# Performance work log

Measured on AMD Instinct MI355X. Metric: run time of the kernel, lower is better.

Reference implementation:

```python
import jax, jax.numpy as jnp
import numpy as np

S_DIM = 4096
N_NODES = 4096
N_EDGES = 32768


def _coarsen(ei_np, N):
    """Integer-only greedy coarsening, faithful to MNGRAPH.forward's while-loop.
    Returns (select order, flattened neighbor indices, segment ids, per-hub
    neighbor counts, forward-fill indices replicating the stale-M behavior for
    empty neighborhoods, and the remapped final edge_index)."""
    ei = ei_np.astype(np.int64).copy()
    I = np.bincount(ei[0], minlength=N)
    O = np.bincount(ei[1], minlength=N)
    order = np.argsort(-(I + O), kind='stable')  # torch.argsort(D, descending=True)
    visits = np.zeros(N, dtype=bool)
    select = []
    nbr_idx, nbr_seg, counts = [], [], []
    while order.size > 0:
        node = int(order[0])
        select.append(node)
        visits[node] = True
        # H = unique neighbors of node in the CURRENT (rewritten) edge_index
        H = np.unique(np.concatenate([ei[1][ei[0] == node], ei[0][ei[1] == node]]))
        visits[H] = True
        order = order[~visits[order]]
        # rewrite: endpoints in H that are not already-selected hubs -> node
        Hn = H[~np.isin(H, np.asarray(select, dtype=np.int64))]
        ei[np.isin(ei, Hn)] = node
        ei = ei[:, ei[0] != ei[1]]  # drop self-loops
        # append reversed edges that are not already present (pair-code isin
        # == the original O(E^2) all/any comparison, computed efficiently)
        code = ei[0] * N + ei[1]
        rcode = ei[1] * N + ei[0]
        new = ~np.isin(rcode, code)
        ei = np.concatenate([ei, ei[::-1][:, new]], axis=1)
        k = len(select) - 1
        nbr_idx.append(H)
        nbr_seg.append(np.full(H.shape[0], k, dtype=np.int64))
        counts.append(H.shape[0])
    select = np.asarray(select, dtype=np.int64)
    sort_sel = np.sort(select)
    ei_out = np.searchsorted(sort_sel, ei)  # compact node ids
    counts = np.asarray(counts, dtype=np.int64)
    # forward-fill: when H is empty the original appends the previous (stale) M
    fill = np.arange(select.shape[0])
    for i in range(select.shape[0]):
        if counts[i] == 0:
            fill[i] = fill[i - 1] if i > 0 else 0
    nbr = np.concatenate(nbr_idx) if nbr_idx else np.zeros(0, np.int64)
    seg = np.concatenate(nbr_seg) if nbr_seg else np.zeros(0, np.int64)
    return select, nbr, seg, counts, fill, ei_out


def setup_inputs() -> dict:
    key = jax.random.key(0)
    k1, k2, k3, k4 = jax.random.split(key, 4)
    x = jax.random.normal(k1, (N_NODES, S_DIM), dtype=jnp.float32)
    edge_index = jax.random.randint(k2, (2, N_EDGES), 0, N_NODES, dtype=jnp.int64)
    bound = float(np.sqrt(6.0 / (1.0 + S_DIM)))  # xavier_uniform on (1, S)
    W1 = jax.random.uniform(k3, (S_DIM,), jnp.float32, -bound, bound)
    W2 = jax.random.uniform(k4, (S_DIM,), jnp.float32, -bound, bound)
    B1 = jnp.zeros((S_DIM,), jnp.float32)
    B2 = jnp.zeros((S_DIM,), jnp.float32)
    return {"x": x, "edge_index": edge_index, "W1": W1, "W2": W2, "B1": B1, "B2": B2}


def reference(x, edge_index, W1, W2, B1, B2):
    N = x.shape[0]
    sel, nbr, seg, counts, fill, ei_out = _coarsen(np.asarray(edge_index), N)
    K = sel.shape[0]
    # Dn = x[n]*W1+B1 for every neighbor of every hub; per-hub mean via segment_sum
    Dn = x[jnp.asarray(nbr)] * W1 + B1                      # [T, S]
    sums = jax.ops.segment_sum(Dn, jnp.asarray(seg), num_segments=K)
    denom = jnp.maximum(jnp.asarray(counts), 1).astype(x.dtype)[:, None]
    mean_Dn = sums / denom                                  # [K, S]
    Dv = x[jnp.asarray(sel)] * W2 + B2                      # [K, S]
    END = jnp.concatenate([Dv, mean_Dn], axis=1)            # [K, 2S]
    END = END[jnp.asarray(fill)]                            # stale-M replication
    return END, jnp.asarray(ei_out)
```

## Files before the change

### kernel.cpp

```cpp
#include <hip/hip_runtime.h>
#include <hip/hip_bf16.h>

#define NT 1024
#define NNODES 4096
#define ECAP 65536

__global__ __launch_bounds__(256)
void zeroBM(int4* __restrict__ bm) {
    bm[(size_t)blockIdx.x * 256 + threadIdx.x] = make_int4(0, 0, 0, 0);
}

__device__ __forceinline__ int blockScanExcl(int v, int* s_w, int* total) {
    const int tid  = threadIdx.x;
    const int lane = tid & 63;
    const int wv   = tid >> 6;
    int x = v;
#pragma unroll
    for (int off = 1; off < 64; off <<= 1) {
        int t = __shfl_up(x, off, 64);
        if (lane >= off) x += t;
    }
    if (lane == 63) s_w[wv] = x;
    __syncthreads();
    if (tid < 16) {
        int y = s_w[tid];
#pragma unroll
        for (int off = 1; off < 16; off <<= 1) {
            int t = __shfl_up(y, off, 16);
            if (tid >= off) y += t;
        }
        s_w[tid] = y;
    }
    __syncthreads();
    int base = wv ? s_w[wv - 1] : 0;
    int tot  = s_w[15];
    __syncthreads();
    *total = tot;
    return base + x - v;
}

__global__ __launch_bounds__(NT, 1)
void phaseA1(const int* __restrict__ ei, int E0,
             int* __restrict__ U, int* __restrict__ V,
             unsigned int* __restrict__ BM,
             int* __restrict__ NBR, int* __restrict__ OTH,
             int* __restrict__ ORDV, int* __restrict__ ROFFG, int* __restrict__ RENDG,
             int* __restrict__ HAND)
{
    __shared__ unsigned short s_order[NNODES];
    __shared__ unsigned char  s_vis[NNODES];
    __shared__ unsigned char  s_rank[NNODES];
    __shared__ unsigned int   s_hb[NNODES / 32];
    __shared__ int s_roff[NNODES];
    __shared__ int s_rend[NNODES];
    __shared__ int s_tmp[NNODES];
    __shared__ int s_mat[64][65];
    __shared__ int s_w[16];
    __shared__ int s_bc[16];

    const int tid = threadIdx.x;

    for (int i = tid; i < NNODES; i += NT) { s_vis[i] = 0; s_tmp[i] = 0; }
    for (int i = tid; i < NNODES / 32; i += NT) s_hb[i] = 0;
    if (tid < 16) s_bc[tid] = 0;
    __syncthreads();

    for (int i = tid; i < E0; i += NT)
        if (ei[2 * i + 1] != 0) s_bc[9] = 1;
    __syncthreads();
    const int is64 = !s_bc[9];

    for (int e = tid; e < E0; e += NT) {
        int uu = ei[is64 ? 2 * e : e];
        int vv = ei[is64 ? 2 * (E0 + e) : (E0 + e)];
        U[e] = uu; V[e] = vv;
        atomicAdd(&s_tmp[uu], 1);
        atomicAdd(&s_tmp[vv], 1);
    }
    __syncthreads();
    for (int n = tid; n < NNODES; n += NT) atomicMax(&s_bc[7], s_tmp[n]);
    __syncthreads();
    const int maxd = s_bc[7];

    if (maxd < 64) {
        const int wv = tid >> 6, lane = tid & 63;
        const unsigned long long ltm = (1ull << lane) - 1ull;
        for (int g = wv; g < 64; g += 16) {
            int n = g * 64 + lane;
            int d = s_tmp[n];
            int rk = 0;
            for (int dd = 0; dd < 64; ++dd) {
                unsigned long long bal = __ballot(d == dd);
                if (lane == 0) s_mat[dd][g] = __popcll(bal);
                if (d == dd) rk = __popcll(bal & ltm);
            }
            s_rank[n] = (unsigned char)rk;
        }
        __syncthreads();
        if (tid < 64) {
            int run = 0;
            for (int g = 0; g < 64; ++g) { int t = s_mat[tid][g]; s_mat[tid][g] = run; run += t; }
            s_mat[tid][64] = run;
        }
        __syncthreads();
        if (tid < 64) {
            int x = s_mat[tid][64];
#pragma unroll
            for (int off = 1; off < 64; off <<= 1) {
                int t = __shfl_up(x, off, 64);
                if (tid >= off) x += t;
            }
            int T = __shfl(x, 63, 64);
            s_mat[tid][64] = T - x;
        }
        __syncthreads();
        for (int g = wv; g < 64; g += 16) {
            int n = g * 64 + lane;
            int d = s_tmp[n];
            int pos = s_mat[d][64] + s_mat[d][g] + (int)s_rank[n];
            s_order[pos] = (unsigned short)n;
        }
        __syncthreads();
    } else {
        for (int d = maxd; d >= 0; --d) {
            int n0 = tid * 4;
            int f0 = (s_tmp[n0] == d), f1 = (s_tmp[n0 + 1] == d);
            int f2 = (s_tmp[n0 + 2] == d), f3 = (s_tmp[n0 + 3] == d);
            int tot;
            int off = blockScanExcl(f0 + f1 + f2 + f3, s_w, &tot);
            int idx = s_bc[4] + off;
            if (f0) s_order[idx++] = (unsigned short)n0;
            if (f1) s_order[idx++] = (unsigned short)(n0 + 1);
            if (f2) s_order[idx++] = (unsigned short)(n0 + 2);
            if (f3) s_order[idx++] = (unsigned short)(n0 + 3);
            __syncthreads();
            if (tid == 0) s_bc[4] += tot;
            __syncthreads();
        }
    }

    if (tid == 0) {
        int nd = s_order[0];
        s_bc[0] = nd; s_vis[nd] = 1;
    }
    __syncthreads();
    {
        const int node = s_bc[0];
        for (int e = tid; e < E0; e += NT) {
            int uu = U[e], vv = V[e];
            if (uu == node) {
                int w = vv; unsigned m = 1u << (w & 31);
                unsigned old = atomicOr(&s_hb[w >> 5], m);
                if (!(old & m)) { int i = atomicAdd(&s_bc[2], 1); s_tmp[i] = w; s_vis[w] = 1; }
            }
            if (vv == node) {
                int w = uu; unsigned m = 1u << (w & 31);
                unsigned old = atomicOr(&s_hb[w >> 5], m);
                if (!(old & m)) { int i = atomicAdd(&s_bc[2], 1); s_tmp[i] = w; s_vis[w] = 1; }
            }
        }
        __syncthreads();
        for (int e = tid; e < E0; e += NT) {
            int uu = U[e];
            if (uu != node && ((s_hb[uu >> 5] >> (uu & 31)) & 1)) U[e] = node;
            int vv = V[e];
            if (vv != node && ((s_hb[vv >> 5] >> (vv & 31)) & 1)) V[e] = node;
        }
        __syncthreads();
    }

    for (int e = tid; e < E0; e += NT) {
        int uu = U[e], vv = V[e];
        if (uu != vv) {
            unsigned code = ((unsigned)uu << 12) | (unsigned)vv;
            atomicOr(&BM[code >> 5], 1u << (code & 31));
        }
    }
    __syncthreads();
    for (int t0 = 0; t0 < E0; t0 += NT * 32) {
        unsigned fm = 0u;
        const int base = t0 + tid * 32;
        for (int j = 0; j < 32; ++j) {
            int e = base + j;
            if (e < E0) {
                int uu = U[e], vv = V[e];
                if (uu != vv) {
                    unsigned rc = ((unsigned)vv << 12) | (unsigned)uu;
                    unsigned old = atomicOr(&BM[rc >> 5], 0u);
                    if (!((old >> (rc & 31)) & 1u)) fm |= (1u << j);
                }
            }
        }
        int tot;
        int off = blockScanExcl(__popc(fm), s_w, &tot);
        int r = s_bc[5] + off;
        unsigned m = fm;
        while (m) {
            int j = __ffs((int)m) - 1; m &= m - 1;
            int e = base + j;
            U[E0 + r] = V[e]; V[E0 + r] = U[e];
            ++r;
        }
        __syncthreads();
        if (tid == 0) s_bc[5] += tot;
        __syncthreads();
    }
    const int E1 = E0 + s_bc[5];

    for (int n = tid; n < NNODES; n += NT) s_roff[n] = 0;
    __syncthreads();
    for (int e = tid; e < E1; e += NT) {
        int uu = U[e], vv = V[e];
        if (uu != vv) atomicAdd(&s_roff[uu], 1);
    }
    __syncthreads();
    {
        int n0 = tid * 4;
        int c0 = s_roff[n0], c1 = s_roff[n0 + 1], c2 = s_roff[n0 + 2], c3 = s_roff[n0 + 3];
        int tot;
        int off = blockScanExcl(c0 + c1 + c2 + c3, s_w, &tot);
        int st = off;
        s_roff[n0] = st;     s_rend[n0] = st;     st += c0;
        s_roff[n0 + 1] = st; s_rend[n0 + 1] = st; st += c1;
        s_roff[n0 + 2] = st; s_rend[n0 + 2] = st; st += c2;
        s_roff[n0 + 3] = st; s_rend[n0 + 3] = st;
    }
    __syncthreads();
    for (int e = tid; e < E1; e += NT) {
        int uu = U[e], vv = V[e];
        if (uu != vv) {
            int p = atomicAdd(&s_rend[uu], 1);
            OTH[p] = vv;
        }
    }
    __syncthreads();
    {
        const int cnt0 = s_bc[2];
        for (int i = tid; i < cnt0; i += NT) NBR[i] = s_tmp[i];
    }
    for (int i = tid; i < NNODES; i += NT) {
        int nd = (int)s_order[i];
        ORDV[i]  = nd | (s_vis[nd] ? 0x8000 : 0);
        ROFFG[i] = s_roff[i];
        RENDG[i] = s_rend[i];
    }
    if (tid == 0) { HAND[0] = E1; HAND[1] = s_bc[2]; HAND[2] = s_bc[0]; }
}

__global__ __launch_bounds__(64, 1)
void phaseA2(const int* __restrict__ OTH, int* __restrict__ NBR,
             const int* __restrict__ ORDV, const int* __restrict__ ROFFG,
             const int* __restrict__ RENDG, const int* __restrict__ HAND,
             int* __restrict__ SEL, int* __restrict__ CNTS,
             int* __restrict__ NST, int* __restrict__ FIL, int* __restrict__ SC,
             int* __restrict__ LABG, int* __restrict__ RNKG)
{
    __shared__ unsigned short s_ord[NNODES];
    __shared__ unsigned int   s_visbits[NNODES / 32];
    __shared__ unsigned int   s_meta[NNODES];
    __shared__ unsigned short s_so[NNODES];
    __shared__ int s_cnt[NNODES];
    __shared__ int s_stamp[NNODES];
    __shared__ int s_roff[NNODES];
    __shared__ int s_rend[NNODES];

    const int ln = threadIdx.x;
    const unsigned long long ltm = (1ull << ln) - 1ull;
    const int cnt0 = HAND[1], hub0 = HAND[2];
    volatile int* vstamp = s_stamp;

    for (int i = ln; i < NNODES / 32; i += 64) s_visbits[i] = 0u;
    for (int i = ln; i < NNODES; i += 64) {
        int ov = ORDV[i];
        int nd = ov & 0x7FFF;
        s_ord[i] = (unsigned short)nd;
        s_meta[nd] = ((unsigned)i << 16) | (unsigned)nd;
        s_roff[i] = ROFFG[i];
        s_rend[i] = RENDG[i];
        s_stamp[i] = 0; s_cnt[i] = 0;
        if (ov & 0x8000) atomicOr(&s_visbits[i >> 5], 1u << (i & 31));
    }
    if (ln == 0) {
        s_meta[hub0] = (unsigned)hub0 | 0x8000u;
        s_so[0] = (unsigned short)hub0;
        s_cnt[0] = cnt0;
    }

    int nc = cnt0;
    int k = 1;

    unsigned lo = 0u, hi = 0u;
    auto reload = [&]() { lo = ~s_visbits[ln]; hi = ~s_visbits[ln + 64]; };
    auto extract = [&]() -> int {
        unsigned long long b = __ballot(lo != 0u);
        if (b) {
            int sl = __ffsll((long long)b) - 1;
            unsigned ww = __shfl(lo, sl, 64);
            if (ln == sl) lo &= lo - 1;
            return sl * 32 + (__ffs((int)ww) - 1);
        }
        b = __ballot(hi != 0u);
        if (b) {
            int sl = __ffsll((long long)b) - 1;
            unsigned ww = __shfl(hi, sl, 64);
            if (ln == sl) hi &= hi - 1;
            return 2048 + sl * 32 + (__ffs((int)ww) - 1);
        }
        return -1;
    };

    auto commitNew = [&](unsigned g, int w, bool nw, unsigned long long bal,
                         unsigned relv) {
        if (nw) {
            NBR[nc + __popcll(bal & ltm)] = w;
            int slot = (int)(g >> 16);
            atomicOr(&s_visbits[slot >> 5], 1u << (slot & 31));
            if (!(g & 0x8000u)) s_meta[w] = relv;
        }
        nc += __popcll(bal);
    };

    auto procFast = [&](int hub, int hslot, int o, unsigned g) {
        const unsigned relv = ((unsigned)hslot << 16) | (unsigned)hub | 0x8000u;
        int w = (o >= 0) ? (int)(g & 0x7FFFu) : hub;
        bool valid = (o >= 0) && (w != hub);
        if (valid) vstamp[w] = ln;
        int r = valid ? vstamp[w] : -1;
        bool nw = valid && (r == ln);
        unsigned long long bal = __ballot(nw);
        commitNew(g, w, nw, bal, relv);
    };

    auto procSlow = [&](int hub, int hslot, int rb, int re, int o0) {
        const unsigned relv = ((unsigned)hslot << 16) | (unsigned)hub | 0x8000u;
        const int key = k << 6;
        int o = o0;
        for (int s0 = rb; s0 < re; s0 += 64) {
            unsigned g = (o >= 0) ? s_meta[o] : 0u;
            int w = (o >= 0) ? (int)(g & 0x7FFFu) : hub;
            bool cnd = (w != hub);
            int old = key;
            if (cnd) old = atomicMax(&s_stamp[w], key);
            bool nw = cnd && (old < key);
            unsigned long long bal = __ballot(nw);
            commitNew(g, w, nw, bal, relv);
            int s1 = s0 + 64;
            o = (s1 + ln < re) ? OTH[s1 + ln] : -1;
        }
    };

    for (;;) {
        reload();
        int sl0 = extract();
        if (sl0 < 0) break;
        int sl1 = extract(), sl2 = -1, sl3 = -1;
        if (sl1 >= 0) { sl2 = extract(); if (sl2 >= 0) sl3 = extract(); }

        int c0 = (int)s_ord[sl0];
        int c1 = (sl1 >= 0) ? (int)s_ord[sl1] : -1;
        int c2 = (sl2 >= 0) ? (int)s_ord[sl2] : -1;
        int c3 = (sl3 >= 0) ? (int)s_ord[sl3] : -1;

        {
            int ms = (ln == 0) ? sl0 : (ln == 1) ? sl1 : (ln == 2) ? sl2 : sl3;
            if (ln < 4 && ms >= 0) atomicOr(&s_visbits[ms >> 5], 1u << (ms & 31));
        }

        int rb0 = s_roff[c0], re0 = s_rend[c0];
        int rb1 = 0, re1 = 0, rb2 = 0, re2 = 0, rb3 = 0, re3 = 0;
        if (c1 >= 0) { rb1 = s_roff[c1]; re1 = s_rend[c1]; }
        if (c2 >= 0) { rb2 = s_roff[c2]; re2 = s_rend[c2]; }
        if (c3 >= 0) { rb3 = s_roff[c3]; re3 = s_rend[c3]; }
        int v0 = (rb0 + ln < re0) ? OTH[rb0 + ln] : -1;
        int v1 = (c1 >= 0 && rb1 + ln < re1) ? OTH[rb1 + ln] : -1;
        int v2 = (c2 >= 0 && rb2 + ln < re2) ? OTH[rb2 + ln] : -1;
        int v3 = (c3 >= 0 && rb3 + ln < re3) ? OTH[rb3 + ln] : -1;

        if (ln == 0) {
            s_meta[c0] = ((unsigned)sl0 << 16) | (unsigned)c0 | 0x8000u;
            s_so[k] = (unsigned short)c0;
        }
        {
            unsigned g0 = (v0 >= 0) ? s_meta[v0] : 0u;
            int begin = nc;
            if (re0 - rb0 <= 64) procFast(c0, sl0, v0, g0);
            else                 procSlow(c0, sl0, rb0, re0, v0);
            if (ln == 0) s_cnt[k] = nc - begin;
            k++;
        }
        if (c1 >= 0) {
            unsigned m1 = s_meta[c1];
            unsigned g1 = (v1 >= 0) ? s_meta[v1] : 0u;
            if ((int)(m1 & 0x7FFFu) == c1) {
                if (ln == 0) {
                    s_meta[c1] = ((unsigned)sl1 << 16) | (unsigned)c1 | 0x8000u;
                    s_so[k] = (unsigned short)c1;
                }
                int begin = nc;
                if (re1 - rb1 <= 64) procFast(c1, sl1, v1, g1);
                else                 procSlow(c1, sl1, rb1, re1, v1);
                if (ln == 0) s_cnt[k] = nc - begin;
                k++;
            }
        }
        if (c2 >= 0) {
            unsigned m2 = s_meta[c2];
            unsigned g2 = (v2 >= 0) ? s_meta[v2] : 0u;
            if ((int)(m2 & 0x7FFFu) == c2) {
                if (ln == 0) {
                    s_meta[c2] = ((unsigned)sl2 << 16) | (unsigned)c2 | 0x8000u;
                    s_so[k] = (unsigned short)c2;
                }
                int begin = nc;
                if (re2 - rb2 <= 64) procFast(c2, sl2, v2, g2);
                else                 procSlow(c2, sl2, rb2, re2, v2);
                if (ln == 0) s_cnt[k] = nc - begin;
                k++;
            }
        }
        if (c3 >= 0) {
            unsigned m3 = s_meta[c3];
            unsigned g3 = (v3 >= 0) ? s_meta[v3] : 0u;
            if ((int)(m3 & 0x7FFFu) == c3) {
                if (ln == 0) {
                    s_meta[c3] = ((unsigned)sl3 << 16) | (unsigned)c3 | 0x8000u;
                    s_so[k] = (unsigned short)c3;
                }
                int begin = nc;
                if (re3 - rb3 <= 64) procFast(c3, sl3, v3, g3);
                else                 procSlow(c3, sl3, rb3, re3, v3);
                if (ln == 0) s_cnt[k] = nc - begin;
                k++;
            }
        }
    }
    const int K = k;

    {
        int base = 0;
        for (int c = 0; c < NNODES / 64; ++c) {
            int n = c * 64 + ln;
            unsigned mv = s_meta[n];
            int f = ((mv & 0x8000u) != 0u) && ((int)(mv & 0x7FFFu) == n);
            unsigned long long b = __ballot(f);
            s_stamp[n] = base + __popcll(b & ltm);
            base += __popcll(b);
        }
    }
    {
        int nb = 0;
        for (int c = 0; c * 64 < K; ++c) {
            int i = c * 64 + ln;
            int cv = (i < K) ? s_cnt[i] : 0;
            int x = cv;
#pragma unroll
            for (int off = 1; off < 64; off <<= 1) {
                int t = __shfl_up(x, off, 64);
                if (ln >= off) x += t;
            }
            if (i < K) { NST[i] = nb + x - cv; CNTS[i] = cv; SEL[i] = (int)s_so[i]; }
            nb += __shfl(x, 63, 64);
        }
    }
    {
        int carry = 0;
        for (int c = 0; c * 64 < K; ++c) {
            int i = c * 64 + ln;
            int f = (i < K) && (s_cnt[i] > 0);
            unsigned long long b = __ballot(f);
            unsigned long long m = b & ((ln == 63) ? ~0ull : ((1ull << (ln + 1)) - 1ull));
            int fil = m ? (c * 64 + 63 - __clzll(m)) : carry;
            if (i < K) FIL[i] = fil;
            carry = b ? (c * 64 + 63 - __clzll(b)) : carry;
        }
    }
    if (ln == 0) SC[0] = K;
    for (int i = ln; i < NNODES; i += 64) {
        LABG[i] = (int)(s_meta[i] & 0x7FFFu);
        RNKG[i] = s_stamp[i];
    }
}

__global__ __launch_bounds__(NT, 1)
void phaseA3(const int* __restrict__ U, const int* __restrict__ V,
             const int* __restrict__ LABG, const int* __restrict__ RNKG,
             const int* __restrict__ HAND, int* __restrict__ SC,
             int* __restrict__ TMP, float* __restrict__ out)
{
    __shared__ unsigned short l_lab[NNODES];
    __shared__ int l_rnk[NNODES];
    __shared__ int s_w[16];
    __shared__ int s_base[1];

    const int tid = threadIdx.x;
    for (int i = tid; i < NNODES; i += NT) {
        l_lab[i] = (unsigned short)LABG[i];
        l_rnk[i] = RNKG[i];
    }
    if (tid == 0) s_base[0] = 0;
    __syncthreads();

    const int E1 = HAND[0];
    const int K  = SC[0];
    const size_t obase = (size_t)K * 8192;

    for (int t0 = 0; t0 < E1; t0 += NT * 64) {
        unsigned long long fm = 0ull;
        const int base = t0 + tid * 64;
        if (base + 64 <= E1) {
            const int4* U4 = (const int4*)(U + base);
            const int4* V4 = (const int4*)(V + base);
#pragma unroll
            for (int q = 0; q < 16; ++q) {
                int4 a = U4[q], b = V4[q];
                int j = q * 4;
                if ((int)l_lab[a.x] != (int)l_lab[b.x]) fm |= 1ull << j;
                if ((int)l_lab[a.y] != (int)l_lab[b.y]) fm |= 1ull << (j + 1);
                if ((int)l_lab[a.z] != (int)l_lab[b.z]) fm |= 1ull << (j + 2);
                if ((int)l_lab[a.w] != (int)l_lab[b.w]) fm |= 1ull << (j + 3);
            }
        } else {
            for (int j = 0; j < 64; ++j) {
                int e = base + j;
                if (e < E1) {
                    if ((int)l_lab[U[e]] != (int)l_lab[V[e]]) fm |= 1ull << j;
                }
            }
        }
        int tot;
        int off = blockScanExcl(__popcll(fm), s_w, &tot);
        int r = s_base[0] + off;
        unsigned long long m = fm;
        while (m) {
            int j = __ffsll((long long)m) - 1; m &= m - 1;
            int e = base + j;
            out[obase + (size_t)r] = (float)l_rnk[(int)l_lab[U[e]]];
            TMP[r] = l_rnk[(int)l_lab[V[e]]];
            ++r;
        }
        __syncthreads();
        if (tid == 0) s_base[0] += tot;
        __syncthreads();
    }
    const int Ef = s_base[0];
    if (tid == 0) SC[1] = Ef;
    for (int r = tid; r < Ef; r += NT)
        out[obase + (size_t)Ef + (size_t)r] = (float)TMP[r];
}

__global__ __launch_bounds__(256, 4)
void phaseB(const float* __restrict__ x,
            const float* __restrict__ W1, const float* __restrict__ W2,
            const float* __restrict__ B1, const float* __restrict__ B2,
            const int* __restrict__ NBR, const int* __restrict__ SEL,
            const int* __restrict__ CNTS, const int* __restrict__ NST,
            const int* __restrict__ FIL, const int* __restrict__ SC,
            float* __restrict__ out)
{
    const int K = SC[0];
    const int k = blockIdx.x;
    if (k >= K) return;
    const int kk   = FIL[k];
    const int node = SEL[kk];
    const int cnt  = CNTS[kk];
    const int st   = NST[kk];
    const int tid  = threadIdx.x;
    const float4* x4 = (const float4*)x;

    float4 acc[4];
#pragma unroll
    for (int j = 0; j < 4; j++) acc[j] = make_float4(0.f, 0.f, 0.f, 0.f);

    for (int r = 0; r < cnt; ++r) {
        const float4* row = x4 + (size_t)NBR[st + r] * 1024;
#pragma unroll
        for (int j = 0; j < 4; j++) {
            float4 t = row[tid + j * 256];
            acc[j].x += t.x; acc[j].y += t.y; acc[j].z += t.z; acc[j].w += t.w;
        }
    }

    const float fc  = (float)cnt;
    const float inv = 1.0f / (float)(cnt > 1 ? cnt : 1);
    const float4* xr = x4 + (size_t)node * 1024;
    float4* o4 = (float4*)(out + (size_t)k * 8192);

#pragma unroll
    for (int j = 0; j < 4; j++) {
        int c = tid + j * 256;
        float4 w1 = ((const float4*)W1)[c], b1 = ((const float4*)B1)[c];
        float4 w2 = ((const float4*)W2)[c], b2 = ((const float4*)B2)[c];
        float4 xv = xr[c];
        float4 pd, pm;
        pd.x = xv.x * w2.x + b2.x;
        pd.y = xv.y * w2.y + b2.y;
        pd.z = xv.z * w2.z + b2.z;
        pd.w = xv.w * w2.w + b2.w;
        pm.x = (acc[j].x * w1.x + fc * b1.x) * inv;
        pm.y = (acc[j].y * w1.y + fc * b1.y) * inv;
        pm.z = (acc[j].z * w1.z + fc * b1.z) * inv;
        pm.w = (acc[j].w * w1.w + fc * b1.w) * inv;
        o4[c] = pd;
        o4[1024 + c] = pm;
    }
}

extern "C" void kernel_launch(void* const* d_in, const int* in_sizes, int n_in,
                              void* d_out, int out_size, void* d_ws, size_t ws_size,
                              hipStream_t stream)
{
    const float* x  = (const float*)d_in[0];
    const int*   ei = (const int*)d_in[1];
    const float* W1 = (const float*)d_in[2];
    const float* W2 = (const float*)d_in[3];
    const float* B1 = (const float*)d_in[4];
    const float* B2 = (const float*)d_in[5];
    const int E0 = in_sizes[1] / 2;

    char* w = (char*)d_ws;
    int* U = (int*)w;
    int* V = U + ECAP;
    unsigned int* BM = (unsigned int*)(V + ECAP);
    int* OTH = (int*)BM;
    int* NBR = OTH + 2 * ECAP;
    int* TMP = NBR + 2 * ECAP;
    char* meta = (char*)BM + (2u << 20);
    int* SEL   = (int*)meta;
    int* CNTS  = SEL  + NNODES;
    int* NST   = CNTS + NNODES;
    int* FIL   = NST  + NNODES;
    int* SC    = FIL  + NNODES;
    int* ORDV  = SC   + 16;
    int* ROFFG = ORDV + NNODES;
    int* RENDG = ROFFG + NNODES;
    int* LABG  = RENDG + NNODES;
    int* RNKG  = LABG + NNODES;
    int* HAND  = RNKG + NNODES;
    float* out = (float*)d_out;

    hipLaunchKernelGGL(zeroBM, dim3(512), dim3(256), 0, stream, (int4*)BM);

    hipLaunchKernelGGL(phaseA1, dim3(1), dim3(NT), 0, stream,
                       ei, E0, U, V, BM, NBR, OTH, ORDV, ROFFG, RENDG, HAND);
    hipLaunchKernelGGL(phaseA2, dim3(1), dim3(64), 0, stream,
                       OTH, NBR, ORDV, ROFFG, RENDG, HAND,
                       SEL, CNTS, NST, FIL, SC, LABG, RNKG);
    hipLaunchKernelGGL(phaseA3, dim3(1), dim3(NT), 0, stream,
                       U, V, LABG, RNKG, HAND, SC, TMP, out);
    hipLaunchKernelGGL(phaseB, dim3(NNODES), dim3(256), 0, stream,
                       x, W1, W2, B1, B2, NBR, SEL, CNTS, NST, FIL, SC, out);
}
```

Measured before the change: 1.005 ms.

## Software-pipeline hub candidate selection in octets with next-batch prefetch

The greedy coarsening loop now pulls eight candidate hubs per iteration instead of four. While the current octet is being processed, it already extracts the next octet's candidates from the visited bitmap and loads their adjacency ranges and first neighbor ids. This is meant to hide LDS and global load latency in the serial single-wave loop behind useful work. In exchange it uses more registers, and it depends on the existing per-candidate s_meta check to reject prefetched nodes that the current octet has just claimed.

```diff
diff --git a/kernel.cpp b/kernel.cpp
--- a/kernel.cpp
+++ b/kernel.cpp
@@ -290,7 +290,6 @@
     int k = 1;
 
     unsigned lo = 0u, hi = 0u;
-    auto reload = [&]() { lo = ~s_visbits[ln]; hi = ~s_visbits[ln + 64]; };
     auto extract = [&]() -> int {
         unsigned long long b = __ballot(lo != 0u);
         if (b) {
@@ -349,91 +348,66 @@
         }
     };
 
+    int nsl0=-1,nsl1=-1,nsl2=-1,nsl3=-1,nsl4=-1,nsl5=-1,nsl6=-1,nsl7=-1;
+    int ncd0=-1,ncd1=-1,ncd2=-1,ncd3=-1,ncd4=-1,ncd5=-1,ncd6=-1,ncd7=-1;
+    int nrb0=0,nrb1=0,nrb2=0,nrb3=0,nrb4=0,nrb5=0,nrb6=0,nrb7=0;
+    int nre0=0,nre1=0,nre2=0,nre3=0,nre4=0,nre5=0,nre6=0,nre7=0;
+    int nv0=-1,nv1=-1,nv2=-1,nv3=-1,nv4=-1,nv5=-1,nv6=-1,nv7=-1;
+
+#define PF_ONE(i) \
+    ncd##i = (nsl##i >= 0) ? (int)s_ord[nsl##i] : -1; \
+    nrb##i = 0; nre##i = 0; \
+    if (ncd##i >= 0) { nrb##i = s_roff[ncd##i]; nre##i = s_rend[ncd##i]; } \
+    nv##i = (ncd##i >= 0 && nrb##i + ln < nre##i) ? OTH[nrb##i + ln] : -1;
+
+#define PREFETCH_OCTET() do { \
+    lo = ~s_visbits[ln]; hi = ~s_visbits[ln + 64]; \
+    nsl0 = extract(); nsl1 = extract(); nsl2 = extract(); nsl3 = extract(); \
+    nsl4 = extract(); nsl5 = extract(); nsl6 = extract(); nsl7 = extract(); \
+    { int ms = (ln==0)?nsl0:(ln==1)?nsl1:(ln==2)?nsl2:(ln==3)?nsl3: \
+               (ln==4)?nsl4:(ln==5)?nsl5:(ln==6)?nsl6:nsl7; \
+      if (ln < 8 && ms >= 0) atomicOr(&s_visbits[ms >> 5], 1u << (ms & 31)); } \
+    PF_ONE(0) PF_ONE(1) PF_ONE(2) PF_ONE(3) PF_ONE(4) PF_ONE(5) PF_ONE(6) PF_ONE(7) \
+} while (0)
+
+#define DO_CAND(CC, SLI, RBI, REI, VI) \
+    if (CC >= 0) { \
+        unsigned mm = s_meta[CC]; \
+        unsigned gg = (VI >= 0) ? s_meta[VI] : 0u; \
+        if ((int)(mm & 0x7FFFu) == CC) { \
+            if (ln == 0) { \
+                s_meta[CC] = ((unsigned)SLI << 16) | (unsigned)CC | 0x8000u; \
+                s_so[k] = (unsigned short)CC; \
+            } \
+            int begin = nc; \
+            if (REI - RBI <= 64) procFast(CC, SLI, VI, gg); \
+            else                 procSlow(CC, SLI, RBI, REI, VI); \
+            if (ln == 0) s_cnt[k] = nc - begin; \
+            k++; \
+        } \
+    }
+
+    PREFETCH_OCTET();
     for (;;) {
-        reload();
-        int sl0 = extract();
-        if (sl0 < 0) break;
-        int sl1 = extract(), sl2 = -1, sl3 = -1;
-        if (sl1 >= 0) { sl2 = extract(); if (sl2 >= 0) sl3 = extract(); }
-
-        int c0 = (int)s_ord[sl0];
-        int c1 = (sl1 >= 0) ? (int)s_ord[sl1] : -1;
-        int c2 = (sl2 >= 0) ? (int)s_ord[sl2] : -1;
-        int c3 = (sl3 >= 0) ? (int)s_ord[sl3] : -1;
-
-        {
-            int ms = (ln == 0) ? sl0 : (ln == 1) ? sl1 : (ln == 2) ? sl2 : sl3;
-            if (ln < 4 && ms >= 0) atomicOr(&s_visbits[ms >> 5], 1u << (ms & 31));
-        }
-
-        int rb0 = s_roff[c0], re0 = s_rend[c0];
-        int rb1 = 0, re1 = 0, rb2 = 0, re2 = 0, rb3 = 0, re3 = 0;
-        if (c1 >= 0) { rb1 = s_roff[c1]; re1 = s_rend[c1]; }
-        if (c2 >= 0) { rb2 = s_roff[c2]; re2 = s_rend[c2]; }
-        if (c3 >= 0) { rb3 = s_roff[c3]; re3 = s_rend[c3]; }
-        int v0 = (rb0 + ln < re0) ? OTH[rb0 + ln] : -1;
-        int v1 = (c1 >= 0 && rb1 + ln < re1) ? OTH[rb1 + ln] : -1;
-        int v2 = (c2 >= 0 && rb2 + ln < re2) ? OTH[rb2 + ln] : -1;
-        int v3 = (c3 >= 0 && rb3 + ln < re3) ? OTH[rb3 + ln] : -1;
-
-        if (ln == 0) {
-            s_meta[c0] = ((unsigned)sl0 << 16) | (unsigned)c0 | 0x8000u;
-            s_so[k] = (unsigned short)c0;
-        }
-        {
-            unsigned g0 = (v0 >= 0) ? s_meta[v0] : 0u;
-            int begin = nc;
-            if (re0 - rb0 <= 64) procFast(c0, sl0, v0, g0);
-            else                 procSlow(c0, sl0, rb0, re0, v0);
-            if (ln == 0) s_cnt[k] = nc - begin;
-            k++;
-        }
-        if (c1 >= 0) {
-            unsigned m1 = s_meta[c1];
-            unsigned g1 = (v1 >= 0) ? s_meta[v1] : 0u;
-            if ((int)(m1 & 0x7FFFu) == c1) {
-                if (ln == 0) {
-                    s_meta[c1] = ((unsigned)sl1 << 16) | (unsigned)c1 | 0x8000u;
-                    s_so[k] = (unsigned short)c1;
-                }
-                int begin = nc;
-                if (re1 - rb1 <= 64) procFast(c1, sl1, v1, g1);
-                else                 procSlow(c1, sl1, rb1, re1, v1);
-                if (ln == 0) s_cnt[k] = nc - begin;
-                k++;
-            }
-        }
-        if (c2 >= 0) {
-            unsigned m2 = s_meta[c2];
-            unsigned g2 = (v2 >= 0) ? s_meta[v2] : 0u;
-            if ((int)(m2 & 0x7FFFu) == c2) {
-                if (ln == 0) {
-                    s_meta[c2] = ((unsigned)sl2 << 16) | (unsigned)c2 | 0x8000u;
-                    s_so[k] = (unsigned short)c2;
-                }
-                int begin = nc;
-                if (re2 - rb2 <= 64) procFast(c2, sl2, v2, g2);
-                else                 procSlow(c2, sl2, rb2, re2, v2);
-                if (ln == 0) s_cnt[k] = nc - begin;
-                k++;
-            }
-        }
-        if (c3 >= 0) {
-            unsigned m3 = s_meta[c3];
-            unsigned g3 = (v3 >= 0) ? s_meta[v3] : 0u;
-            if ((int)(m3 & 0x7FFFu) == c3) {
-                if (ln == 0) {
-                    s_meta[c3] = ((unsigned)sl3 << 16) | (unsigned)c3 | 0x8000u;
-                    s_so[k] = (unsigned short)c3;
-                }
-                int begin = nc;
-                if (re3 - rb3 <= 64) procFast(c3, sl3, v3, g3);
-                else                 procSlow(c3, sl3, rb3, re3, v3);
-                if (ln == 0) s_cnt[k] = nc - begin;
-                k++;
-            }
-        }
-    }
+        int c0=ncd0,c1=ncd1,c2=ncd2,c3=ncd3,c4=ncd4,c5=ncd5,c6=ncd6,c7=ncd7;
+        int t0=nsl0,t1=nsl1,t2=nsl2,t3=nsl3,t4=nsl4,t5=nsl5,t6=nsl6,t7=nsl7;
+        int a0=nrb0,a1=nrb1,a2=nrb2,a3=nrb3,a4=nrb4,a5=nrb5,a6=nrb6,a7=nrb7;
+        int e0=nre0,e1=nre1,e2=nre2,e3=nre3,e4=nre4,e5=nre5,e6=nre6,e7=nre7;
+        int v0=nv0,v1=nv1,v2=nv2,v3=nv3,v4=nv4,v5=nv5,v6=nv6,v7=nv7;
+        if (c0 < 0) break;
+        PREFETCH_OCTET();
+        DO_CAND(c0, t0, a0, e0, v0);
+        DO_CAND(c1, t1, a1, e1, v1);
+        DO_CAND(c2, t2, a2, e2, v2);
+        DO_CAND(c3, t3, a3, e3, v3);
+        DO_CAND(c4, t4, a4, e4, v4);
+        DO_CAND(c5, t5, a5, e5, v5);
+        DO_CAND(c6, t6, a6, e6, v6);
+        DO_CAND(c7, t7, a7, e7, v7);
+    }
+#undef DO_CAND
+#undef PREFETCH_OCTET
+#undef PF_ONE
     const int K = k;
 
     {
```

After: 1.043 ms. 1.04x slower.
